# Performance work log

Measured on AMD Instinct MI355X. Metric: run time of the kernel, lower is better.

## Reference

```python
import jax, jax.numpy as jnp
import numpy as np

N, E, F, D, G = 50000, 800000, 64, 64, 512
BN_EPS = 1e-5


def setup_inputs() -> dict:
    key = jax.random.key(0)
    ks = jax.random.split(key, 12)
    inp = {
        "x": jax.random.normal(ks[0], (N, F), dtype=jnp.float32),
        "edge_index": jax.random.randint(ks[1], (2, E), 0, N, dtype=jnp.int32),
        "batch": jnp.sort(jax.random.randint(ks[2], (N,), 0, G, dtype=jnp.int32)),
    }
    s = 0.05
    inp.update({
        "w1_a": jax.random.normal(ks[3], (F, D), jnp.float32) * s, "b1_a": jnp.zeros((D,), jnp.float32),
        "w1_b": jax.random.normal(ks[4], (D, D), jnp.float32) * s, "b1_b": jnp.zeros((D,), jnp.float32),
        "g1": jnp.ones((D,), jnp.float32), "be1": jnp.zeros((D,), jnp.float32),
        "w2_a": jax.random.normal(ks[5], (D, D), jnp.float32) * s, "b2_a": jnp.zeros((D,), jnp.float32),
        "w2_b": jax.random.normal(ks[6], (D, D), jnp.float32) * s, "b2_b": jnp.zeros((D,), jnp.float32),
        "g2": jnp.ones((D,), jnp.float32), "be2": jnp.zeros((D,), jnp.float32),
        "w3_a": jax.random.normal(ks[7], (D, D), jnp.float32) * s, "b3_a": jnp.zeros((D,), jnp.float32),
        "w3_b": jax.random.normal(ks[8], (D, D), jnp.float32) * s, "b3_b": jnp.zeros((D,), jnp.float32),
        "g3": jnp.ones((D,), jnp.float32), "be3": jnp.zeros((D,), jnp.float32),
        "w_lin0": jax.random.normal(ks[9], (D, 2 * D), jnp.float32) * s, "b_lin0": jnp.zeros((2 * D,), jnp.float32),
        "w_fc1": jax.random.normal(ks[10], (2 * D, D), jnp.float32) * s, "b_fc1": jnp.zeros((D,), jnp.float32),
    })
    return inp


def _gin_bn_layer(h, edge_index, w_a, b_a, w_b, b_b, gamma, beta):
    # GINConv (eps=0): nn(x + sum_{j->i} x_j); message = x[src] scattered to dst
    agg = jax.ops.segment_sum(h[edge_index[0]], edge_index[1], num_segments=h.shape[0])
    z = agg + h
    z = jnp.maximum(z @ w_a + b_a, 0.0) @ w_b + b_b  # inner MLP
    z = jnp.maximum(z, 0.0)                           # F.relu after conv
    mean = jnp.mean(z, axis=0)                        # BatchNorm1d, training stats
    var = jnp.mean((z - mean) ** 2, axis=0)
    return (z - mean) * jax.lax.rsqrt(var + BN_EPS) * gamma + beta


def reference(x, edge_index, batch,
              w1_a, b1_a, w1_b, b1_b, g1, be1,
              w2_a, b2_a, w2_b, b2_b, g2, be2,
              w3_a, b3_a, w3_b, b3_b, g3, be3,
              w_lin0, b_lin0, w_fc1, b_fc1):
    h = _gin_bn_layer(x, edge_index, w1_a, b1_a, w1_b, b1_b, g1, be1)
    h = _gin_bn_layer(h, edge_index, w2_a, b2_a, w2_b, b2_b, g2, be2)
    h = _gin_bn_layer(h, edge_index, w3_a, b3_a, w3_b, b3_b, g3, be3)
    xpool = jax.ops.segment_sum(h, batch, num_segments=G)  # global_add_pool [G, D]
    out = xpool @ w_lin0 + b_lin0                           # GINEncoder.lin0 -> [G, 2D]
    out = jnp.maximum(out @ w_fc1 + b_fc1, 0.0)             # relu(fc1); fc2 output is discarded (show_embedding=True)
    return out
```

## Files before the change

### kernel.cpp

```cpp
#include <hip/hip_runtime.h>

#define NN 50000
#define EE 800000
#define DD 64
#define GG 512
#define TILES 782
#define SCAN_BLOCKS 98

typedef __attribute__((ext_vector_type(8))) short short8;
typedef __attribute__((ext_vector_type(4))) float f32x4;

__device__ __forceinline__ float b2f(unsigned short u) {
    union { unsigned int i; float f; } c;
    c.i = ((unsigned int)u) << 16;
    return c.f;
}
__device__ __forceinline__ unsigned short f2b(float f) {
    union { float f; unsigned int i; } c;
    c.f = f;
    const unsigned int r = c.i + 0x7FFFu + ((c.i >> 16) & 1u);
    return (unsigned short)(r >> 16);
}
__device__ __forceinline__ int rfl(int v) { return __builtin_amdgcn_readfirstlane(v); }

__global__ __launch_bounds__(256) void prep_kernel(const float* __restrict__ x,
                                                   unsigned short* __restrict__ xbf,
                                                   int* __restrict__ counts,
                                                   float* __restrict__ zblock) {
    const int tid = blockIdx.x * 256 + threadIdx.x;
    if (tid < 800000) {
        const float4 v = ((const float4*)x)[tid];
        ushort4 o;
        o.x = f2b(v.x); o.y = f2b(v.y); o.z = f2b(v.z); o.w = f2b(v.w);
        ((ushort4*)xbf)[tid] = o;
    } else if (tid < 812500) {
        ((int4*)counts)[tid - 800000] = make_int4(0, 0, 0, 0);
    } else if (tid < 821464) {
        ((float4*)zblock)[tid - 812500] = make_float4(0.f, 0.f, 0.f, 0.f);
    }
}

__global__ __launch_bounds__(256) void wprep_kernel(const float* __restrict__ w0,
                                                    const float* __restrict__ w1,
                                                    const float* __restrict__ w2,
                                                    const float* __restrict__ w3,
                                                    const float* __restrict__ w4,
                                                    const float* __restrict__ w5,
                                                    unsigned short* __restrict__ out) {
    const float* ws[6] = {w0, w1, w2, w3, w4, w5};
    const float* w = ws[blockIdx.x];
    unsigned short* o = out + blockIdx.x * 4096;
    #pragma unroll
    for (int it = 0; it < 2; ++it) {
        const int idx = it * 256 + threadIdx.x;
        const int fid = idx >> 6, lane = idx & 63;
        const int kt = fid >> 2, nt = fid & 3;
        const int kbase = kt * 32 + (lane >> 4) * 8;
        const int n = nt * 16 + (lane & 15);
        #pragma unroll
        for (int j = 0; j < 8; ++j)
            o[idx * 8 + j] = f2b(w[(kbase + j) * 64 + n]);
    }
}

__global__ __launch_bounds__(256) void hist_kernel(const int* __restrict__ ei,
                                                   int* __restrict__ counts) {
    const int e = blockIdx.x * blockDim.x + threadIdx.x;
    if (e < EE) atomicAdd(&counts[ei[EE + e]], 1);
}

__global__ __launch_bounds__(512) void scan1_kernel(const int* __restrict__ counts,
                                                    int* __restrict__ scanned,
                                                    int* __restrict__ bsum) {
    __shared__ int buf[512];
    const int i = blockIdx.x * 512 + threadIdx.x;
    const int v = (i < NN) ? counts[i] : 0;
    buf[threadIdx.x] = v;
    __syncthreads();
    for (int off = 1; off < 512; off <<= 1) {
        const int add = (threadIdx.x >= off) ? buf[threadIdx.x - off] : 0;
        __syncthreads();
        buf[threadIdx.x] += add;
        __syncthreads();
    }
    if (i < NN) scanned[i] = buf[threadIdx.x] - v;
    if (threadIdx.x == 511) bsum[blockIdx.x] = buf[511];
}

__global__ __launch_bounds__(512) void scan2_kernel(const int* __restrict__ scanned,
                                                    const int* __restrict__ bsum,
                                                    int* __restrict__ rowptr,
                                                    int* __restrict__ cursor) {
    __shared__ int red[128];
    if (threadIdx.x < 128)
        red[threadIdx.x] = (threadIdx.x < blockIdx.x) ? bsum[threadIdx.x] : 0;
    __syncthreads();
    for (int off = 64; off > 0; off >>= 1) {
        if (threadIdx.x < off) red[threadIdx.x] += red[threadIdx.x + off];
        __syncthreads();
    }
    const int offset = red[0];
    const int i = blockIdx.x * 512 + threadIdx.x;
    if (i < NN) {
        const int p = scanned[i] + offset;
        rowptr[i] = p;
        cursor[i] = p;
    }
    if (blockIdx.x == 0 && threadIdx.x == 0) rowptr[NN] = EE;
}

__global__ __launch_bounds__(256) void fill_kernel(const int* __restrict__ ei,
                                                   int* __restrict__ cursor,
                                                   int* __restrict__ col) {
    const int cls = blockIdx.x & 7;
    const int chunk = blockIdx.x >> 3;
    const int e0 = chunk * 3125;
    for (int e = e0 + threadIdx.x; e < e0 + 3125; e += 256) {
        const int dst = ei[EE + e];
        if (dst / 6250 == cls) {
            const int pos = atomicAdd(&cursor[dst], 1);
            col[pos] = ei[e];
        }
    }
}

__global__ __launch_bounds__(256, 4) void gather_kernel(const unsigned short* __restrict__ hin,
                                                        const int* __restrict__ rowptr,
                                                        const int* __restrict__ col,
                                                        const float* __restrict__ ss,
                                                        const int apply,
                                                        unsigned short* __restrict__ z) {
    const int wv = (blockIdx.x * 256 + threadIdx.x) >> 6;
    const int lane = threadIdx.x & 63;
    const int row = rfl(wv);
    if (row >= NN) return;
    const float scl = apply ? ss[lane] : 1.0f;
    const float sft = apply ? ss[64 + lane] : 0.0f;

    const int beg = rfl(rowptr[row]);
    const int end = rfl(rowptr[row + 1]);
    const int deg = end - beg;
    float a[8];
    #pragma unroll
    for (int i = 0; i < 8; ++i) a[i] = 0.f;
    a[0] = b2f(hin[row * 64 + lane]);

    if (deg <= 16) {
        const int safeb = (beg < EE) ? beg : 0;
        int c[16];
        #pragma unroll
        for (int i = 0; i < 16; ++i) {
            const int jj = (i < deg) ? (beg + i) : safeb;
            c[i] = rfl(col[jj]);
        }
        float hv[16];
        #pragma unroll
        for (int i = 0; i < 16; ++i) hv[i] = b2f(hin[c[i] * 64 + lane]);
        #pragma unroll
        for (int i = 0; i < 16; ++i) a[i & 7] += (i < deg) ? hv[i] : 0.f;
    } else if (deg <= 32) {
        int c[32];
        #pragma unroll
        for (int i = 0; i < 32; ++i) {
            const int jj = (i < deg) ? (beg + i) : beg;
            c[i] = rfl(col[jj]);
        }
        float hv[32];
        #pragma unroll
        for (int i = 0; i < 32; ++i) hv[i] = b2f(hin[c[i] * 64 + lane]);
        #pragma unroll
        for (int i = 0; i < 32; ++i) a[i & 7] += (i < deg) ? hv[i] : 0.f;
    } else {
        int j = beg;
        for (; j + 16 <= end; j += 16) {
            int c[16];
            #pragma unroll
            for (int i = 0; i < 16; ++i) c[i] = rfl(col[j + i]);
            float hv[16];
            #pragma unroll
            for (int i = 0; i < 16; ++i) hv[i] = b2f(hin[c[i] * 64 + lane]);
            #pragma unroll
            for (int i = 0; i < 16; ++i) a[i & 7] += hv[i];
        }
        if (j < end) {
            int c[16];
            #pragma unroll
            for (int i = 0; i < 16; ++i) {
                const int jj = (j + i < end) ? (j + i) : beg;
                c[i] = rfl(col[jj]);
            }
            float hv[16];
            #pragma unroll
            for (int i = 0; i < 16; ++i) hv[i] = b2f(hin[c[i] * 64 + lane]);
            #pragma unroll
            for (int i = 0; i < 16; ++i) a[i & 7] += (j + i < end) ? hv[i] : 0.f;
        }
    }
    const float sum = ((a[0] + a[1]) + (a[2] + a[3])) + ((a[4] + a[5]) + (a[6] + a[7]));
    z[row * 64 + lane] = f2b(fmaf(sum, scl, (float)(deg + 1) * sft));
}

__global__ __launch_bounds__(256, 2) void mlp_kernel(const unsigned short* __restrict__ z,
                                                     const unsigned short* __restrict__ wfa,
                                                     const float* __restrict__ ba,
                                                     const unsigned short* __restrict__ wfb,
                                                     const float* __restrict__ bb,
                                                     unsigned short* __restrict__ tout,
                                                     float* __restrict__ stats) {
    __shared__ unsigned short ldsT[4][16][72];
    __shared__ float red[512];

    const int wave = threadIdx.x >> 6;
    const int lane = threadIdx.x & 63;
    const int quad = lane >> 4;
    const int l15 = lane & 15;
    const int rowbase = blockIdx.x * 64 + wave * 16;
    const bool valid = rowbase < NN;

    short8 wA[8], wB[8];
    #pragma unroll
    for (int f = 0; f < 8; ++f) {
        wA[f] = *(const short8*)(wfa + (f * 64 + lane) * 8);
        wB[f] = *(const short8*)(wfb + (f * 64 + lane) * 8);
    }
    float biasA[4], biasB[4];
    #pragma unroll
    for (int nt = 0; nt < 4; ++nt) {
        biasA[nt] = ba[nt * 16 + l15];
        biasB[nt] = bb[nt * 16 + l15];
    }

    const int arow = valid ? (rowbase + l15) : 0;
    const short8 a0 = *(const short8*)(z + arow * 64 + quad * 8);
    const short8 a1 = *(const short8*)(z + arow * 64 + 32 + quad * 8);

    f32x4 acc[4];
    #pragma unroll
    for (int nt = 0; nt < 4; ++nt) {
        f32x4 c = {0.f, 0.f, 0.f, 0.f};
        c = __builtin_amdgcn_mfma_f32_16x16x32_bf16(a0, wA[nt], c, 0, 0, 0);
        c = __builtin_amdgcn_mfma_f32_16x16x32_bf16(a1, wA[4 + nt], c, 0, 0, 0);
        acc[nt] = c;
    }
    #pragma unroll
    for (int nt = 0; nt < 4; ++nt)
        #pragma unroll
        for (int r = 0; r < 4; ++r)
            ldsT[wave][quad * 4 + r][nt * 16 + l15] =
                f2b(fmaxf(acc[nt][r] + biasA[nt], 0.f));

    const short8 y0 = *(const short8*)(&ldsT[wave][l15][quad * 8]);
    const short8 y1 = *(const short8*)(&ldsT[wave][l15][32 + quad * 8]);

    #pragma unroll
    for (int nt = 0; nt < 4; ++nt) {
        f32x4 c = {0.f, 0.f, 0.f, 0.f};
        c = __builtin_amdgcn_mfma_f32_16x16x32_bf16(y0, wB[nt], c, 0, 0, 0);
        c = __builtin_amdgcn_mfma_f32_16x16x32_bf16(y1, wB[4 + nt], c, 0, 0, 0);
        acc[nt] = c;
    }
    #pragma unroll
    for (int nt = 0; nt < 4; ++nt)
        #pragma unroll
        for (int r = 0; r < 4; ++r)
            ldsT[wave][quad * 4 + r][nt * 16 + l15] =
                f2b(fmaxf(acc[nt][r] + biasB[nt], 0.f));

    {
        float s = 0.f, sq = 0.f;
        if (valid) {
            #pragma unroll 4
            for (int r = 0; r < 16; ++r) {
                const float v = b2f(ldsT[wave][r][lane]);
                s += v;
                sq += v * v;
            }
        }
        red[wave * 128 + lane] = s;
        red[wave * 128 + 64 + lane] = sq;
    }
    __syncthreads();

    if (threadIdx.x < 128) {
        const float tot = red[threadIdx.x] + red[128 + threadIdx.x] +
                          red[256 + threadIdx.x] + red[384 + threadIdx.x];
        atomicAdd(&stats[(blockIdx.x & 7) * 128 + threadIdx.x], tot);
    }

    #pragma unroll
    for (int m = 0; m < 4; ++m) {
        const int g = m * 256 + threadIdx.x;
        const int r = g >> 4;
        const int f4 = (g & 15) * 4;
        const int grow = blockIdx.x * 64 + r;
        if (grow < NN)
            *(ushort4*)(tout + grow * 64 + f4) =
                *(const ushort4*)(&ldsT[r >> 4][r & 15][f4]);
    }
}

__global__ __launch_bounds__(128) void finalize_kernel(const float* __restrict__ stats,
                                                       const float* __restrict__ g,
                                                       const float* __restrict__ be,
                                                       float* __restrict__ ss) {
    __shared__ float red[128];
    const int f = threadIdx.x;
    float tot = 0.f;
    #pragma unroll
    for (int k = 0; k < 8; ++k) tot += stats[k * 128 + f];
    red[f] = tot;
    __syncthreads();
    if (f < 64) {
        const float mean = red[f] * (1.0f / NN);
        const float var = red[64 + f] * (1.0f / NN) - mean * mean;
        const float scl = g[f] * rsqrtf(var + 1e-5f);
        ss[f] = scl;
        ss[64 + f] = be[f] - mean * scl;
    }
}

__global__ __launch_bounds__(256) void pool_kernel(const unsigned short* __restrict__ t,
                                                   const int* __restrict__ batch,
                                                   const float* __restrict__ ss,
                                                   float* __restrict__ xpool) {
    const int wv = (blockIdx.x * 256 + threadIdx.x) >> 6;
    const int lane = threadIdx.x & 63;
    const int r0 = wv * 64;
    if (r0 >= NN) return;
    const int r1 = min(r0 + 64, NN);
    const float scl = ss[lane];
    const float sft = ss[64 + lane];
    int gprev = batch[r0];
    float acc = 0.f;
    for (int r = r0; r < r1; ++r) {
        const int g = batch[r];
        if (g != gprev) {
            __hip_atomic_fetch_add(&xpool[gprev * 64 + lane], acc,
                                   __ATOMIC_RELAXED, __HIP_MEMORY_SCOPE_AGENT);
            acc = 0.f;
            gprev = g;
        }
        acc += fmaf(b2f(t[r * 64 + lane]), scl, sft);
    }
    __hip_atomic_fetch_add(&xpool[gprev * 64 + lane], acc,
                           __ATOMIC_RELAXED, __HIP_MEMORY_SCOPE_AGENT);
}

__global__ __launch_bounds__(128) void head_kernel(const float* __restrict__ xpool,
                                                   const float* __restrict__ w0,
                                                   const float* __restrict__ b0,
                                                   const float* __restrict__ w1,
                                                   const float* __restrict__ b1,
                                                   float* __restrict__ out) {
    __shared__ float xp[64];
    __shared__ float midl[128];
    const int g = blockIdx.x;
    const int t = threadIdx.x;
    if (t < 64) xp[t] = xpool[g * 64 + t];
    __syncthreads();
    float acc = b0[t];
    #pragma unroll 8
    for (int k = 0; k < 64; ++k) acc = fmaf(xp[k], w0[k * 128 + t], acc);
    midl[t] = acc;
    __syncthreads();
    if (t < 64) {
        float a2 = b1[t];
        #pragma unroll 8
        for (int k = 0; k < 128; ++k) a2 = fmaf(midl[k], w1[k * 64 + t], a2);
        out[g * 64 + t] = fmaxf(a2, 0.f);
    }
}

extern "C" void kernel_launch(void* const* d_in, const int* in_sizes, int n_in,
                              void* d_out, int out_size, void* d_ws, size_t ws_size,
                              hipStream_t stream) {
    const float* x = (const float*)d_in[0];
    const int* ei = (const int*)d_in[1];
    const int* batch = (const int*)d_in[2];

    int* ibase   = (int*)d_ws;
    int* counts  = ibase;
    int* scanned = ibase + 50000;
    int* rowptr  = ibase + 100000;
    int* cursor  = ibase + 150004;
    int* bsum    = ibase + 200004;
    int* col     = ibase + 200132;
    float* fbase = (float*)d_ws + 1000192;
    float* stats = fbase;
    float* xpool = stats + 3072;
    float* ss    = xpool + 32768 + 16;
    unsigned short* zbf  = (unsigned short*)(fbase + 35856 + 128);
    unsigned short* xbf  = zbf + 3200000;
    unsigned short* t0bf = xbf + 3200000;
    unsigned short* t1bf = t0bf + 3200000;
    unsigned short* wfrag = t1bf + 3200000;

    prep_kernel<<<(821464 + 255) / 256, 256, 0, stream>>>(x, xbf, counts, stats);
    wprep_kernel<<<6, 256, 0, stream>>>(
        (const float*)d_in[3], (const float*)d_in[5],
        (const float*)d_in[9], (const float*)d_in[11],
        (const float*)d_in[15], (const float*)d_in[17], wfrag);
    hist_kernel<<<(EE + 255) / 256, 256, 0, stream>>>(ei, counts);
    scan1_kernel<<<SCAN_BLOCKS, 512, 0, stream>>>(counts, scanned, bsum);
    scan2_kernel<<<SCAN_BLOCKS, 512, 0, stream>>>(scanned, bsum, rowptr, cursor);
    fill_kernel<<<2048, 256, 0, stream>>>(ei, cursor, col);

    const unsigned short* hcur = xbf;
    unsigned short* touts[3] = {t0bf, t1bf, t0bf};
    for (int l = 0; l < 3; ++l) {
        const float* ba = (const float*)d_in[3 + l * 6 + 1];
        const float* bb = (const float*)d_in[3 + l * 6 + 3];
        const float* ga = (const float*)d_in[3 + l * 6 + 4];
        const float* be = (const float*)d_in[3 + l * 6 + 5];

        gather_kernel<<<12500, 256, 0, stream>>>(hcur, rowptr, col, ss, l > 0, zbf);
        mlp_kernel<<<TILES, 256, 0, stream>>>(zbf,
                                              wfrag + (l * 2 + 0) * 4096, ba,
                                              wfrag + (l * 2 + 1) * 4096, bb,
                                              touts[l], stats + l * 1024);
        finalize_kernel<<<1, 128, 0, stream>>>(stats + l * 1024, ga, be, ss);
        hcur = touts[l];
    }

    pool_kernel<<<(TILES + 3) / 4, 256, 0, stream>>>(t0bf, batch, ss, xpool);
    head_kernel<<<GG, 128, 0, stream>>>(
        xpool, (const float*)d_in[21], (const float*)d_in[22],
        (const float*)d_in[23], (const float*)d_in[24], (float*)d_out);
}
```

Baseline: 322.1 us.

## Fuse neighbor gather into MLP kernel and fold small prep/finalize launches

The separate gather kernel is removed. Each MLP block now aggregates neighbor rows directly into MFMA A-fragments, with each lane handling one row and reading 16-byte bf16 chunks, so the bf16 z buffer no longer makes a round trip through global memory. Weight preparation is merged into prep_kernel as extra blocks, and the last layer's finalize is folded into pool_kernel, which recomputes the BN scale and shift itself. These changes cut launches and memory traffic. The trade-off is that lanes handling rows of different degree now loop to the wave's maximum degree, wasting work to divergence. The gather also runs with lower occupancy and fewer parallel memory requests than the old one-wave-per-row scheme.

After: 317.1 us. About the same (-1.5%).

```diff
diff --git a/kernel.cpp b/kernel.cpp
--- a/kernel.cpp
+++ b/kernel.cpp
@@ -21,12 +21,36 @@
     const unsigned int r = c.i + 0x7FFFu + ((c.i >> 16) & 1u);
     return (unsigned short)(r >> 16);
 }
-__device__ __forceinline__ int rfl(int v) { return __builtin_amdgcn_readfirstlane(v); }
 
 __global__ __launch_bounds__(256) void prep_kernel(const float* __restrict__ x,
                                                    unsigned short* __restrict__ xbf,
                                                    int* __restrict__ counts,
-                                                   float* __restrict__ zblock) {
+                                                   float* __restrict__ zblock,
+                                                   const float* __restrict__ w0,
+                                                   const float* __restrict__ w1,
+                                                   const float* __restrict__ w2,
+                                                   const float* __restrict__ w3,
+                                                   const float* __restrict__ w4,
+                                                   const float* __restrict__ w5,
+                                                   unsigned short* __restrict__ wfrag) {
+    if (blockIdx.x >= 3209) {
+        const float* ws[6] = {w0, w1, w2, w3, w4, w5};
+        const int wi = blockIdx.x - 3209;
+        const float* w = ws[wi];
+        unsigned short* o = wfrag + wi * 4096;
+        #pragma unroll
+        for (int it = 0; it < 2; ++it) {
+            const int idx = it * 256 + threadIdx.x;
+            const int fid = idx >> 6, lane = idx & 63;
+            const int kt = fid >> 2, nt = fid & 3;
+            const int kbase = kt * 32 + (lane >> 4) * 8;
+            const int n = nt * 16 + (lane & 15);
+            #pragma unroll
+            for (int j = 0; j < 8; ++j)
+                o[idx * 8 + j] = f2b(w[(kbase + j) * 64 + n]);
+        }
+        return;
+    }
     const int tid = blockIdx.x * 256 + threadIdx.x;
     if (tid < 800000) {
         const float4 v = ((const float4*)x)[tid];
@@ -35,31 +59,8 @@
         ((ushort4*)xbf)[tid] = o;
     } else if (tid < 812500) {
         ((int4*)counts)[tid - 800000] = make_int4(0, 0, 0, 0);
-    } else if (tid < 821464) {
+    } else if (tid < 821460) {
         ((float4*)zblock)[tid - 812500] = make_float4(0.f, 0.f, 0.f, 0.f);
-    }
-}
-
-__global__ __launch_bounds__(256) void wprep_kernel(const float* __restrict__ w0,
-                                                    const float* __restrict__ w1,
-                                                    const float* __restrict__ w2,
-                                                    const float* __restrict__ w3,
-                                                    const float* __restrict__ w4,
-                                                    const float* __restrict__ w5,
-                                                    unsigned short* __restrict__ out) {
-    const float* ws[6] = {w0, w1, w2, w3, w4, w5};
-    const float* w = ws[blockIdx.x];
-    unsigned short* o = out + blockIdx.x * 4096;
-    #pragma unroll
-    for (int it = 0; it < 2; ++it) {
-        const int idx = it * 256 + threadIdx.x;
-        const int fid = idx >> 6, lane = idx & 63;
-        const int kt = fid >> 2, nt = fid & 3;
-        const int kbase = kt * 32 + (lane >> 4) * 8;
-        const int n = nt * 16 + (lane & 15);
-        #pragma unroll
-        for (int j = 0; j < 8; ++j)
-            o[idx * 8 + j] = f2b(w[(kbase + j) * 64 + n]);
     }
 }
 
@@ -124,89 +125,17 @@
     }
 }
 
-__global__ __launch_bounds__(256, 4) void gather_kernel(const unsigned short* __restrict__ hin,
-                                                        const int* __restrict__ rowptr,
-                                                        const int* __restrict__ col,
-                                                        const float* __restrict__ ss,
-                                                        const int apply,
-                                                        unsigned short* __restrict__ z) {
-    const int wv = (blockIdx.x * 256 + threadIdx.x) >> 6;
-    const int lane = threadIdx.x & 63;
-    const int row = rfl(wv);
-    if (row >= NN) return;
-    const float scl = apply ? ss[lane] : 1.0f;
-    const float sft = apply ? ss[64 + lane] : 0.0f;
-
-    const int beg = rfl(rowptr[row]);
-    const int end = rfl(rowptr[row + 1]);
-    const int deg = end - beg;
-    float a[8];
-    #pragma unroll
-    for (int i = 0; i < 8; ++i) a[i] = 0.f;
-    a[0] = b2f(hin[row * 64 + lane]);
-
-    if (deg <= 16) {
-        const int safeb = (beg < EE) ? beg : 0;
-        int c[16];
-        #pragma unroll
-        for (int i = 0; i < 16; ++i) {
-            const int jj = (i < deg) ? (beg + i) : safeb;
-            c[i] = rfl(col[jj]);
-        }
-        float hv[16];
-        #pragma unroll
-        for (int i = 0; i < 16; ++i) hv[i] = b2f(hin[c[i] * 64 + lane]);
-        #pragma unroll
-        for (int i = 0; i < 16; ++i) a[i & 7] += (i < deg) ? hv[i] : 0.f;
-    } else if (deg <= 32) {
-        int c[32];
-        #pragma unroll
-        for (int i = 0; i < 32; ++i) {
-            const int jj = (i < deg) ? (beg + i) : beg;
-            c[i] = rfl(col[jj]);
-        }
-        float hv[32];
-        #pragma unroll
-        for (int i = 0; i < 32; ++i) hv[i] = b2f(hin[c[i] * 64 + lane]);
-        #pragma unroll
-        for (int i = 0; i < 32; ++i) a[i & 7] += (i < deg) ? hv[i] : 0.f;
-    } else {
-        int j = beg;
-        for (; j + 16 <= end; j += 16) {
-            int c[16];
-            #pragma unroll
-            for (int i = 0; i < 16; ++i) c[i] = rfl(col[j + i]);
-            float hv[16];
-            #pragma unroll
-            for (int i = 0; i < 16; ++i) hv[i] = b2f(hin[c[i] * 64 + lane]);
-            #pragma unroll
-            for (int i = 0; i < 16; ++i) a[i & 7] += hv[i];
-        }
-        if (j < end) {
-            int c[16];
-            #pragma unroll
-            for (int i = 0; i < 16; ++i) {
-                const int jj = (j + i < end) ? (j + i) : beg;
-                c[i] = rfl(col[jj]);
-            }
-            float hv[16];
-            #pragma unroll
-            for (int i = 0; i < 16; ++i) hv[i] = b2f(hin[c[i] * 64 + lane]);
-            #pragma unroll
-            for (int i = 0; i < 16; ++i) a[i & 7] += (j + i < end) ? hv[i] : 0.f;
-        }
-    }
-    const float sum = ((a[0] + a[1]) + (a[2] + a[3])) + ((a[4] + a[5]) + (a[6] + a[7]));
-    z[row * 64 + lane] = f2b(fmaf(sum, scl, (float)(deg + 1) * sft));
-}
-
-__global__ __launch_bounds__(256, 2) void mlp_kernel(const unsigned short* __restrict__ z,
-                                                     const unsigned short* __restrict__ wfa,
-                                                     const float* __restrict__ ba,
-                                                     const unsigned short* __restrict__ wfb,
-                                                     const float* __restrict__ bb,
-                                                     unsigned short* __restrict__ tout,
-                                                     float* __restrict__ stats) {
+__global__ __launch_bounds__(256, 2) void fmlp_kernel(const unsigned short* __restrict__ hin,
+                                                      const int* __restrict__ rowptr,
+                                                      const int* __restrict__ col,
+                                                      const float* __restrict__ ss,
+                                                      const int apply,
+                                                      const unsigned short* __restrict__ wfa,
+                                                      const float* __restrict__ ba,
+                                                      const unsigned short* __restrict__ wfb,
+                                                      const float* __restrict__ bb,
+                                                      unsigned short* __restrict__ tout,
+                                                      float* __restrict__ stats) {
     __shared__ unsigned short ldsT[4][16][72];
     __shared__ float red[512];
 
@@ -215,7 +144,59 @@
     const int quad = lane >> 4;
     const int l15 = lane & 15;
     const int rowbase = blockIdx.x * 64 + wave * 16;
-    const bool valid = rowbase < NN;
+    const bool wvalid = rowbase < NN;
+    const int row = rowbase + l15;
+    const int rp = (row < NN) ? row : (NN - 1);
+    const int beg = rowptr[rp];
+    const int deg = (row < NN) ? (rowptr[rp + 1] - beg) : 0;
+
+    float facc[16];
+    {
+        const short8 h0 = *(const short8*)(hin + rp * 64 + quad * 8);
+        const short8 h1 = *(const short8*)(hin + rp * 64 + 32 + quad * 8);
+        const float ms = (row < NN) ? 1.f : 0.f;
+        #pragma unroll
+        for (int j = 0; j < 8; ++j) {
+            facc[j]     = b2f((unsigned short)h0[j]) * ms;
+            facc[8 + j] = b2f((unsigned short)h1[j]) * ms;
+        }
+    }
+    int md = deg;
+    #pragma unroll
+    for (int off = 32; off; off >>= 1) md = max(md, __shfl_xor(md, off));
+    for (int i = 0; i < md; i += 2) {
+        const int j0 = (i < deg) ? (beg + i) : 0;
+        const int j1 = (i + 1 < deg) ? (beg + i + 1) : 0;
+        const int s0 = col[j0];
+        const int s1 = col[j1];
+        const short8 p0 = *(const short8*)(hin + s0 * 64 + quad * 8);
+        const short8 p1 = *(const short8*)(hin + s0 * 64 + 32 + quad * 8);
+        const short8 q0 = *(const short8*)(hin + s1 * 64 + quad * 8);
+        const short8 q1 = *(const short8*)(hin + s1 * 64 + 32 + quad * 8);
+        const float m0 = (i < deg) ? 1.f : 0.f;
+        const float m1 = (i + 1 < deg) ? 1.f : 0.f;
+        #pragma unroll
+        for (int j = 0; j < 8; ++j) {
+            facc[j]     += b2f((unsigned short)p0[j]) * m0;
+            facc[j]     += b2f((unsigned short)q0[j]) * m1;
+            facc[8 + j] += b2f((unsigned short)p1[j]) * m0;
+            facc[8 + j] += b2f((unsigned short)q1[j]) * m1;
+        }
+    }
+
+    short8 a0, a1;
+    {
+        const float degp1 = (float)(deg + 1);
+        #pragma unroll
+        for (int j = 0; j < 8; ++j) {
+            const float sc0 = apply ? ss[quad * 8 + j] : 1.f;
+            const float sf0 = apply ? ss[64 + quad * 8 + j] : 0.f;
+            const float sc1 = apply ? ss[32 + quad * 8 + j] : 1.f;
+            const float sf1 = apply ? ss[96 + quad * 8 + j] : 0.f;
+            a0[j] = (short)f2b(fmaf(facc[j], sc0, degp1 * sf0));
+            a1[j] = (short)f2b(fmaf(facc[8 + j], sc1, degp1 * sf1));
+        }
+    }
 
     short8 wA[8], wB[8];
     #pragma unroll
@@ -229,10 +210,6 @@
         biasA[nt] = ba[nt * 16 + l15];
         biasB[nt] = bb[nt * 16 + l15];
     }
-
-    const int arow = valid ? (rowbase + l15) : 0;
-    const short8 a0 = *(const short8*)(z + arow * 64 + quad * 8);
-    const short8 a1 = *(const short8*)(z + arow * 64 + 32 + quad * 8);
 
     f32x4 acc[4];
     #pragma unroll
@@ -268,7 +245,7 @@
 
     {
         float s = 0.f, sq = 0.f;
-        if (valid) {
+        if (wvalid) {
             #pragma unroll 4
             for (int r = 0; r < 16; ++r) {
                 const float v = b2f(ldsT[wave][r][lane]);
@@ -321,15 +298,27 @@
 
 __global__ __launch_bounds__(256) void pool_kernel(const unsigned short* __restrict__ t,
                                                    const int* __restrict__ batch,
-                                                   const float* __restrict__ ss,
+                                                   const float* __restrict__ stats,
+                                                   const float* __restrict__ ga,
+                                                   const float* __restrict__ be,
                                                    float* __restrict__ xpool) {
     const int wv = (blockIdx.x * 256 + threadIdx.x) >> 6;
     const int lane = threadIdx.x & 63;
+
+    float s = 0.f, sq = 0.f;
+    #pragma unroll
+    for (int k = 0; k < 8; ++k) {
+        s += stats[k * 128 + lane];
+        sq += stats[k * 128 + 64 + lane];
+    }
+    const float mean = s * (1.0f / NN);
+    const float var = sq * (1.0f / NN) - mean * mean;
+    const float scl = ga[lane] * rsqrtf(var + 1e-5f);
+    const float sft = be[lane] - mean * scl;
+
     const int r0 = wv * 64;
     if (r0 >= NN) return;
     const int r1 = min(r0 + 64, NN);
-    const float scl = ss[lane];
-    const float sft = ss[64 + lane];
     int gprev = batch[r0];
     float acc = 0.f;
     for (int r = r0; r < r1; ++r) {
@@ -388,18 +377,17 @@
     float* fbase = (float*)d_ws + 1000192;
     float* stats = fbase;
     float* xpool = stats + 3072;
-    float* ss    = xpool + 32768 + 16;
-    unsigned short* zbf  = (unsigned short*)(fbase + 35856 + 128);
-    unsigned short* xbf  = zbf + 3200000;
+    float* ss    = fbase + 35840;
+    unsigned short* xbf  = (unsigned short*)(fbase + 36096);
     unsigned short* t0bf = xbf + 3200000;
     unsigned short* t1bf = t0bf + 3200000;
     unsigned short* wfrag = t1bf + 3200000;
 
-    prep_kernel<<<(821464 + 255) / 256, 256, 0, stream>>>(x, xbf, counts, stats);
-    wprep_kernel<<<6, 256, 0, stream>>>(
-        (const float*)d_in[3], (const float*)d_in[5],
-        (const float*)d_in[9], (const float*)d_in[11],
-        (const float*)d_in[15], (const float*)d_in[17], wfrag);
+    prep_kernel<<<3215, 256, 0, stream>>>(x, xbf, counts, stats,
+                                          (const float*)d_in[3], (const float*)d_in[5],
+                                          (const float*)d_in[9], (const float*)d_in[11],
+                                          (const float*)d_in[15], (const float*)d_in[17],
+                                          wfrag);
     hist_kernel<<<(EE + 255) / 256, 256, 0, stream>>>(ei, counts);
     scan1_kernel<<<SCAN_BLOCKS, 512, 0, stream>>>(counts, scanned, bsum);
     scan2_kernel<<<SCAN_BLOCKS, 512, 0, stream>>>(scanned, bsum, rowptr, cursor);
@@ -413,16 +401,18 @@
         const float* ga = (const float*)d_in[3 + l * 6 + 4];
         const float* be = (const float*)d_in[3 + l * 6 + 5];
 
-        gather_kernel<<<12500, 256, 0, stream>>>(hcur, rowptr, col, ss, l > 0, zbf);
-        mlp_kernel<<<TILES, 256, 0, stream>>>(zbf,
-                                              wfrag + (l * 2 + 0) * 4096, ba,
-                                              wfrag + (l * 2 + 1) * 4096, bb,
-                                              touts[l], stats + l * 1024);
-        finalize_kernel<<<1, 128, 0, stream>>>(stats + l * 1024, ga, be, ss);
+        fmlp_kernel<<<TILES, 256, 0, stream>>>(hcur, rowptr, col, ss, l > 0,
+                                               wfrag + (l * 2 + 0) * 4096, ba,
+                                               wfrag + (l * 2 + 1) * 4096, bb,
+                                               touts[l], stats + l * 1024);
+        if (l < 2)
+            finalize_kernel<<<1, 128, 0, stream>>>(stats + l * 1024, ga, be, ss);
         hcur = touts[l];
     }
 
-    pool_kernel<<<(TILES + 3) / 4, 256, 0, stream>>>(t0bf, batch, ss, xpool);
+    pool_kernel<<<(TILES + 3) / 4, 256, 0, stream>>>(
+        t0bf, batch, stats + 2048,
+        (const float*)d_in[19], (const float*)d_in[20], xpool);
     head_kernel<<<GG, 128, 0, stream>>>(
         xpool, (const float*)d_in[21], (const float*)d_in[22],
         (const float*)d_in[23], (const float*)d_in[24], (float*)d_out);
```
